# Optimization experiments

Hardware: AMD Instinct MI355X
Metric: run time of the kernel (lower is better)

The kernel has to match this reference:

```python
import jax, jax.numpy as jnp
import numpy as np

B, N = 32, 1024
CD, GD, HD, OD = 896, 384, 256, 1280  # cluster/geometric/hidden/output dims
EPS_BN = 1e-5


def _w(k, out_d, in_d):
    return jax.random.normal(k, (in_d, out_d), jnp.float32) / np.sqrt(in_d)


def setup_inputs() -> dict:
    key = jax.random.key(0)
    ks = jax.random.split(key, 12)
    return {
        "cluster_features": jax.random.normal(ks[0], (B, N, CD), jnp.float32),
        "geometric_features": jax.random.normal(ks[1], (B, N, GD), jnp.float32),
        "cluster_weights": jax.random.uniform(ks[2], (B, N, N), jnp.float32),
        # linear projections (stored as [in, out])
        "Wq": _w(ks[3], HD, CD), "bq": jnp.zeros((HD,), jnp.float32),
        "Wk": _w(ks[4], HD, GD), "bk": jnp.zeros((HD,), jnp.float32),
        "Wv": _w(ks[5], HD, GD), "bv": jnp.zeros((HD,), jnp.float32),
        "Wcp": _w(ks[6], OD // 2, CD), "bcp": jnp.zeros((OD // 2,), jnp.float32),
        "Wgp": _w(ks[7], OD // 2, HD), "bgp": jnp.zeros((OD // 2,), jnp.float32),
        # fusion head: Linear -> BN(eval) -> ReLU -> (Dropout=identity) -> Linear
        "Wf1": _w(ks[8], OD, OD), "bf1": jnp.zeros((OD,), jnp.float32),
        "bn_gamma": jnp.ones((OD,), jnp.float32),
        "bn_beta": jnp.zeros((OD,), jnp.float32),
        "bn_mean": jnp.zeros((OD,), jnp.float32),
        "bn_var": jnp.ones((OD,), jnp.float32),
        "Wf2": _w(ks[9], OD, OD), "bf2": jnp.zeros((OD,), jnp.float32),
    }


def reference(cluster_features, geometric_features, cluster_weights,
              Wq, bq, Wk, bk, Wv, bv, Wcp, bcp, Wgp, bgp,
              Wf1, bf1, bn_gamma, bn_beta, bn_mean, bn_var, Wf2, bf2):
    Q = cluster_features @ Wq + bq            # [B,N,HD]
    K = geometric_features @ Wk + bk          # [B,N,HD]
    V = geometric_features @ Wv + bv          # [B,N,HD]

    scale = 1.0 / np.sqrt(Q.shape[-1]).astype(np.float32)
    scores = jnp.einsum('bnd,bmd->bnm', Q, K) * scale  # [B,N,N]
    scores = scores + jnp.log(cluster_weights + 1e-8)
    attn = jax.nn.softmax(scores, axis=-1)             # [B,N,N]
    attended = jnp.einsum('bnm,bmd->bnd', attn, V)     # [B,N,HD]

    cluster_pooled = jnp.mean(cluster_features, axis=1)  # [B,CD]
    geom_pooled = jnp.mean(attended, axis=1)             # [B,HD]

    combined = jnp.concatenate([cluster_pooled @ Wcp + bcp,
                                geom_pooled @ Wgp + bgp], axis=-1)  # [B,OD]

    h = combined @ Wf1 + bf1
    h = (h - bn_mean) * jax.lax.rsqrt(bn_var + EPS_BN) * bn_gamma + bn_beta  # BN eval
    h = jax.nn.relu(h)  # dropout is identity at inference
    out = h @ Wf2 + bf2
    return out, attn
```

## Files before the change

### kernel.cpp

```cpp
#include <hip/hip_runtime.h>
#include <stdint.h>

typedef short    v8s  __attribute__((ext_vector_type(8)));
typedef float    v4f  __attribute__((ext_vector_type(4)));
typedef unsigned short u16x8 __attribute__((ext_vector_type(8)));
typedef unsigned short ushort_t;

#define NB   32
#define NN   1024
#define CD   896
#define GD   384
#define HD   256
#define OD   1280
#define SP   1028

static __device__ __forceinline__ unsigned short f2bf(float f) {
    union { float f; unsigned u; } v; v.f = f;
    unsigned r = v.u + 0x7fffu + ((v.u >> 16) & 1u);
    return (unsigned short)(r >> 16);
}

static __device__ __forceinline__ v4f mfma16(v8s a, v8s b, v4f c) {
    return __builtin_amdgcn_mfma_f32_16x16x32_bf16(a, b, c, 0, 0, 0);
}

static __device__ __forceinline__ void stage_cvt16(const float* __restrict__ src, ushort_t* dst) {
    const float4* s4 = (const float4*)src;
    float4 f0 = s4[0], f1 = s4[1], f2 = s4[2], f3 = s4[3];
    u16x8 p0, p1;
    p0[0]=f2bf(f0.x); p0[1]=f2bf(f0.y); p0[2]=f2bf(f0.z); p0[3]=f2bf(f0.w);
    p0[4]=f2bf(f1.x); p0[5]=f2bf(f1.y); p0[6]=f2bf(f1.z); p0[7]=f2bf(f1.w);
    p1[0]=f2bf(f2.x); p1[1]=f2bf(f2.y); p1[2]=f2bf(f2.z); p1[3]=f2bf(f2.w);
    p1[4]=f2bf(f3.x); p1[5]=f2bf(f3.y); p1[6]=f2bf(f3.z); p1[7]=f2bf(f3.w);
    *(u16x8*)dst = p0;
    *(u16x8*)(dst + 8) = p1;
}

static __device__ __forceinline__ void stage_copy16(const ushort_t* __restrict__ src, ushort_t* dst) {
    const u16x8* s = (const u16x8*)src;
    u16x8 a = s[0], b = s[1];
    *(u16x8*)dst = a;
    *(u16x8*)(dst + 8) = b;
}

__global__ void convw_kernel(const float* __restrict__ W, ushort_t* __restrict__ Wt, int Kd) {
    int idx = blockIdx.x * 256 + threadIdx.x;
    int k = idx >> 8, n = idx & 255;
    Wt[(size_t)n * Kd + k] = f2bf(W[idx]);
}

__global__ void zero_kernel(float* __restrict__ p, int n) {
    int i = blockIdx.x * 256 + threadIdx.x;
    if (i < n) p[i] = 0.f;
}

__global__ void pool_kernel(const float* __restrict__ cf, float* __restrict__ pooled) {
    int b = blockIdx.y, chunk = blockIdx.x, t = threadIdx.x;
    if (t >= 224) return;
    const float4* p = (const float4*)(cf + (size_t)(b * NN + chunk * 128) * CD) + t;
    float4 s = {0.f, 0.f, 0.f, 0.f};
    #pragma unroll 4
    for (int n = 0; n < 128; ++n) {
        float4 v = p[(size_t)n * 224];
        s.x += v.x; s.y += v.y; s.z += v.z; s.w += v.w;
    }
    const float sc = 1.f / 1024.f;
    float* dst = pooled + b * CD + t * 4;
    atomicAdd(dst + 0, s.x * sc);
    atomicAdd(dst + 1, s.y * sc);
    atomicAdd(dst + 2, s.z * sc);
    atomicAdd(dst + 3, s.w * sc);
}

template<int KD>
__global__ __launch_bounds__(256) void proj_kernel(
    const float* __restrict__ A, const ushort_t* __restrict__ Wt,
    const float* __restrict__ bias, ushort_t* __restrict__ C)
{
    __shared__ ushort_t lA[128 * 40];
    __shared__ ushort_t lB[128 * 40];
    const int tid  = threadIdx.x;
    const int m0   = blockIdx.x * 128;
    const int n0   = blockIdx.y * 128;
    const int lane = tid & 63, wave = tid >> 6;
    const int l15  = lane & 15, quad = lane >> 4;
    const int wrow = (wave >> 1) * 64, wcol = (wave & 1) * 64;
    const int srow = tid >> 1, shalf = tid & 1;

    v4f acc[4][4];
    #pragma unroll
    for (int i = 0; i < 4; ++i)
        #pragma unroll
        for (int j = 0; j < 4; ++j) acc[i][j] = v4f{0.f, 0.f, 0.f, 0.f};

    for (int kt = 0; kt < KD / 32; ++kt) {
        stage_cvt16(A + (size_t)(m0 + srow) * KD + kt * 32 + shalf * 16,
                    &lA[srow * 40 + shalf * 16]);
        stage_copy16(Wt + (size_t)(n0 + srow) * KD + kt * 32 + shalf * 16,
                     &lB[srow * 40 + shalf * 16]);
        __syncthreads();
        v8s af[4], bfr[4];
        #pragma unroll
        for (int rt = 0; rt < 4; ++rt) af[rt]  = *(const v8s*)&lA[(wrow + rt * 16 + l15) * 40 + quad * 8];
        #pragma unroll
        for (int ct = 0; ct < 4; ++ct) bfr[ct] = *(const v8s*)&lB[(wcol + ct * 16 + l15) * 40 + quad * 8];
        #pragma unroll
        for (int rt = 0; rt < 4; ++rt)
            #pragma unroll
            for (int ct = 0; ct < 4; ++ct)
                acc[rt][ct] = mfma16(af[rt], bfr[ct], acc[rt][ct]);
        __syncthreads();
    }

    #pragma unroll
    for (int ct = 0; ct < 4; ++ct) {
        int col = n0 + wcol + ct * 16 + l15;
        float bv = bias[col];
        #pragma unroll
        for (int rt = 0; rt < 4; ++rt)
            #pragma unroll
            for (int r = 0; r < 4; ++r) {
                int row = m0 + wrow + rt * 16 + quad * 4 + r;
                C[(size_t)row * 256 + col] = f2bf(acc[rt][ct][r] + bv);
            }
    }
}

__global__ __launch_bounds__(512) void attn_kernel(
    const ushort_t* __restrict__ Qb, const ushort_t* __restrict__ Kb,
    const float* __restrict__ cw,
    float* __restrict__ attn, float* __restrict__ colsum)
{
    __shared__ float S[32 * SP];
    const int bat = blockIdx.x;
    const int m0  = blockIdx.y * 32;
    const int tid = threadIdx.x;
    const int lane = tid & 63, wave = tid >> 6;
    const int l15 = lane & 15, quad = lane >> 4;

    v8s af[2][8];
    #pragma unroll
    for (int rt = 0; rt < 2; ++rt)
        #pragma unroll
        for (int ks = 0; ks < 8; ++ks)
            af[rt][ks] = *(const v8s*)(Qb + (size_t)(bat * NN + m0 + rt * 16 + l15) * HD + ks * 32 + quad * 8);

    const int n0w = wave * 128;
    #pragma unroll 2
    for (int ct = 0; ct < 8; ++ct) {
        const int col = n0w + ct * 16 + l15;
        v8s bfr[8];
        #pragma unroll
        for (int ks = 0; ks < 8; ++ks)
            bfr[ks] = *(const v8s*)(Kb + (size_t)(bat * NN + col) * HD + ks * 32 + quad * 8);
        float w0[4], w1[4];
        const size_t cwb = ((size_t)bat << 20) + col;
        #pragma unroll
        for (int r = 0; r < 4; ++r) {
            w0[r] = cw[cwb + (size_t)(m0 + quad * 4 + r) * NN];
            w1[r] = cw[cwb + (size_t)(m0 + 16 + quad * 4 + r) * NN];
        }
        v4f acc0 = {0.f, 0.f, 0.f, 0.f}, acc1 = {0.f, 0.f, 0.f, 0.f};
        #pragma unroll
        for (int ks = 0; ks < 8; ++ks) {
            acc0 = mfma16(af[0][ks], bfr[ks], acc0);
            acc1 = mfma16(af[1][ks], bfr[ks], acc1);
        }
        #pragma unroll
        for (int r = 0; r < 4; ++r) {
            const int row0 = quad * 4 + r;
            S[row0 * SP + col]        = acc0[r] * 0.0625f + __logf(w0[r] + 1e-8f);
            S[(16 + row0) * SP + col] = acc1[r] * 0.0625f + __logf(w1[r] + 1e-8f);
        }
    }
    __syncthreads();

    float4 cs[4];
    #pragma unroll
    for (int i = 0; i < 4; ++i) cs[i] = float4{0.f, 0.f, 0.f, 0.f};

    #pragma unroll 1
    for (int rr = 0; rr < 4; ++rr) {
        const int row = wave * 4 + rr;
        float* Srow = &S[row * SP];
        float4 v[4];
        #pragma unroll
        for (int i = 0; i < 4; ++i) v[i] = *(float4*)(Srow + i * 256 + lane * 4);
        float m = -1e30f;
        #pragma unroll
        for (int i = 0; i < 4; ++i)
            m = fmaxf(m, fmaxf(fmaxf(v[i].x, v[i].y), fmaxf(v[i].z, v[i].w)));
        #pragma unroll
        for (int off = 1; off <= 32; off <<= 1) m = fmaxf(m, __shfl_xor(m, off));
        float s = 0.f;
        #pragma unroll
        for (int i = 0; i < 4; ++i) {
            v[i].x = __expf(v[i].x - m); v[i].y = __expf(v[i].y - m);
            v[i].z = __expf(v[i].z - m); v[i].w = __expf(v[i].w - m);
            s += v[i].x + v[i].y + v[i].z + v[i].w;
        }
        #pragma unroll
        for (int off = 1; off <= 32; off <<= 1) s += __shfl_xor(s, off);
        const float inv = 1.0f / s;
        float* grow = attn + ((size_t)bat << 20) + (size_t)(m0 + row) * NN;
        #pragma unroll
        for (int i = 0; i < 4; ++i) {
            v[i].x *= inv; v[i].y *= inv; v[i].z *= inv; v[i].w *= inv;
            *(float4*)(grow + i * 256 + lane * 4) = v[i];
            cs[i].x += v[i].x; cs[i].y += v[i].y; cs[i].z += v[i].z; cs[i].w += v[i].w;
        }
    }

    __syncthreads();
    #pragma unroll
    for (int i = 0; i < 4; ++i)
        *(float4*)&S[wave * 1024 + i * 256 + lane * 4] = cs[i];
    __syncthreads();
    {
        const int c = tid * 2;
        float s0 = 0.f, s1 = 0.f;
        #pragma unroll
        for (int w = 0; w < 8; ++w) {
            float2 p = *(const float2*)&S[w * 1024 + c];
            s0 += p.x; s1 += p.y;
        }
        atomicAdd(&colsum[(size_t)bat * NN + c + 0], s0);
        atomicAdd(&colsum[(size_t)bat * NN + c + 1], s1);
    }
}

__global__ __launch_bounds__(192) void wpool_kernel(
    const float* __restrict__ gf, const float* __restrict__ colsum,
    float* __restrict__ gws)
{
    const int b = blockIdx.y, m0 = blockIdx.x * 128, t = threadIdx.x;
    const float2* base = (const float2*)(gf + (size_t)(b * NN + m0) * GD);
    const float* wbase = colsum + (size_t)b * NN + m0;
    float sx = 0.f, sy = 0.f;
    #pragma unroll 4
    for (int m = 0; m < 128; ++m) {
        const float w = wbase[m] * (1.f / 1024.f);
        float2 v = base[(size_t)m * (GD / 2) + t];
        sx += w * v.x; sy += w * v.y;
    }
    atomicAdd(&gws[b * GD + 2 * t + 0], sx);
    atomicAdd(&gws[b * GD + 2 * t + 1], sy);
}

__global__ __launch_bounds__(256) void vproj_kernel(
    const float* __restrict__ gws, const float* __restrict__ Wv,
    const float* __restrict__ bv, float* __restrict__ gpool)
{
    const int b = blockIdx.x, d = threadIdx.x;
    const float* g = gws + (size_t)b * GD;
    float acc = bv[d];
    #pragma unroll 8
    for (int k = 0; k < GD; ++k) acc += g[k] * Wv[(size_t)k * HD + d];
    gpool[b * HD + d] = acc;
}

__global__ void tail1_kernel(const float* __restrict__ pooled, const float* __restrict__ gpool,
                             const float* __restrict__ Wcp, const float* __restrict__ bcp,
                             const float* __restrict__ Wgp, const float* __restrict__ bgp,
                             float* __restrict__ combined)
{
    int idx = blockIdx.x * 256 + threadIdx.x;
    int b = idx / OD, c = idx % OD;
    float acc;
    if (c < 640) {
        acc = bcp[c];
        const float* a = pooled + b * CD;
        for (int k = 0; k < CD; ++k) acc += a[k] * Wcp[k * 640 + c];
    } else {
        int c2 = c - 640;
        acc = bgp[c2];
        const float* g = gpool + b * HD;
        for (int k = 0; k < HD; ++k) acc += g[k] * Wgp[k * 640 + c2];
    }
    combined[idx] = acc;
}

__global__ void tail2_kernel(const float* __restrict__ combined, const float* __restrict__ Wf1,
                             const float* __restrict__ bf1,
                             const float* __restrict__ g, const float* __restrict__ be,
                             const float* __restrict__ mn, const float* __restrict__ vr,
                             float* __restrict__ h)
{
    int idx = blockIdx.x * 256 + threadIdx.x;
    int b = idx / OD, c = idx % OD;
    float acc = bf1[c];
    const float* a = combined + b * OD;
    for (int k = 0; k < OD; ++k) acc += a[k] * Wf1[k * OD + c];
    float x = (acc - mn[c]) * rsqrtf(vr[c] + 1e-5f) * g[c] + be[c];
    h[idx] = fmaxf(x, 0.f);
}

__global__ void tail3_kernel(const float* __restrict__ h, const float* __restrict__ Wf2,
                             const float* __restrict__ bf2, float* __restrict__ out)
{
    int idx = blockIdx.x * 256 + threadIdx.x;
    int b = idx / OD, c = idx % OD;
    float acc = bf2[c];
    const float* a = h + b * OD;
    for (int k = 0; k < OD; ++k) acc += a[k] * Wf2[k * OD + c];
    out[idx] = acc;
}

extern "C" void kernel_launch(void* const* d_in, const int* in_sizes, int n_in,
                              void* d_out, int out_size, void* d_ws, size_t ws_size,
                              hipStream_t stream)
{
    const float* cf  = (const float*)d_in[0];
    const float* gf  = (const float*)d_in[1];
    const float* cw  = (const float*)d_in[2];
    const float* Wq  = (const float*)d_in[3];  const float* bq  = (const float*)d_in[4];
    const float* Wk  = (const float*)d_in[5];  const float* bk  = (const float*)d_in[6];
    const float* Wv  = (const float*)d_in[7];  const float* bv  = (const float*)d_in[8];
    const float* Wcp = (const float*)d_in[9];  const float* bcp = (const float*)d_in[10];
    const float* Wgp = (const float*)d_in[11]; const float* bgp = (const float*)d_in[12];
    const float* Wf1 = (const float*)d_in[13]; const float* bf1 = (const float*)d_in[14];
    const float* bng = (const float*)d_in[15]; const float* bnb = (const float*)d_in[16];
    const float* bnm = (const float*)d_in[17]; const float* bnv = (const float*)d_in[18];
    const float* Wf2 = (const float*)d_in[19]; const float* bf2 = (const float*)d_in[20];

    float* out  = (float*)d_out;
    float* attn = out + NB * OD;

    char* w = (char*)d_ws;
    ushort_t* Qb  = (ushort_t*)w; w += (size_t)NB * NN * HD * 2;
    ushort_t* Kb  = (ushort_t*)w; w += (size_t)NB * NN * HD * 2;
    ushort_t* Wqt = (ushort_t*)w; w += (size_t)HD * CD * 2;
    ushort_t* Wkt = (ushort_t*)w; w += (size_t)HD * GD * 2;
    float* pooled   = (float*)w; w += (size_t)NB * CD * 4;
    float* gpool    = (float*)w; w += (size_t)NB * HD * 4;
    float* colsum   = (float*)w; w += (size_t)NB * NN * 4;
    float* gws      = (float*)w; w += (size_t)NB * GD * 4;
    float* combined = (float*)w; w += (size_t)NB * OD * 4;
    float* hbuf     = (float*)w; w += (size_t)NB * OD * 4;

    const int nz = NB * (CD + HD + NN + GD);
    zero_kernel<<<dim3((nz + 255) / 256), dim3(256), 0, stream>>>(pooled, nz);
    convw_kernel<<<dim3(CD), dim3(256), 0, stream>>>(Wq, Wqt, CD);
    convw_kernel<<<dim3(GD), dim3(256), 0, stream>>>(Wk, Wkt, GD);
    pool_kernel<<<dim3(8, 32), dim3(256), 0, stream>>>(cf, pooled);

    proj_kernel<CD><<<dim3(256, 2), dim3(256), 0, stream>>>(cf, Wqt, bq, Qb);
    proj_kernel<GD><<<dim3(256, 2), dim3(256), 0, stream>>>(gf, Wkt, bk, Kb);

    attn_kernel<<<dim3(32, 32), dim3(512), 0, stream>>>(Qb, Kb, cw, attn, colsum);

    wpool_kernel<<<dim3(8, 32), dim3(192), 0, stream>>>(gf, colsum, gws);
    vproj_kernel<<<dim3(32), dim3(256), 0, stream>>>(gws, Wv, bv, gpool);

    tail1_kernel<<<dim3(160), dim3(256), 0, stream>>>(pooled, gpool, Wcp, bcp, Wgp, bgp, combined);
    tail2_kernel<<<dim3(160), dim3(256), 0, stream>>>(combined, Wf1, bf1, bng, bnb, bnm, bnv, hbuf);
    tail3_kernel<<<dim3(160), dim3(256), 0, stream>>>(hbuf, Wf2, bf2, out);
}
```

Baseline: 754.8 us.

## Keep attention scores in registers and add ILP to reduction kernels

The attention kernel no longer stages the 32x1024 score tile in a ~128KB shared buffer. Each 256-thread block now handles 16 rows, keeps all scores in MFMA accumulators, preloads the log-weights into them, and does max and sum through shuffles plus a tiny shared reduction. The point is higher occupancy and fewer LDS round trips. The cost is that attn stores become strided 4-byte writes instead of float4 rows, and colsum atomics rise to one per column per block. Separately, the pool, wpool, vproj and tail kernels split their sums across multiple accumulators for more ILP, and pool uses twice as many blocks.

```diff
diff --git a/kernel.cpp b/kernel.cpp
--- a/kernel.cpp
+++ b/kernel.cpp
@@ -12,7 +12,6 @@
 #define GD   384
 #define HD   256
 #define OD   1280
-#define SP   1028
 
 static __device__ __forceinline__ unsigned short f2bf(float f) {
     union { float f; unsigned u; } v; v.f = f;
@@ -57,19 +56,25 @@
 __global__ void pool_kernel(const float* __restrict__ cf, float* __restrict__ pooled) {
     int b = blockIdx.y, chunk = blockIdx.x, t = threadIdx.x;
     if (t >= 224) return;
-    const float4* p = (const float4*)(cf + (size_t)(b * NN + chunk * 128) * CD) + t;
-    float4 s = {0.f, 0.f, 0.f, 0.f};
-    #pragma unroll 4
-    for (int n = 0; n < 128; ++n) {
-        float4 v = p[(size_t)n * 224];
-        s.x += v.x; s.y += v.y; s.z += v.z; s.w += v.w;
+    const float4* p = (const float4*)(cf + (size_t)(b * NN + chunk * 64) * CD) + t;
+    float4 s0{0,0,0,0}, s1{0,0,0,0}, s2{0,0,0,0}, s3{0,0,0,0};
+    #pragma unroll 1
+    for (int n = 0; n < 64; n += 4) {
+        float4 v0 = p[(size_t)(n + 0) * 224];
+        float4 v1 = p[(size_t)(n + 1) * 224];
+        float4 v2 = p[(size_t)(n + 2) * 224];
+        float4 v3 = p[(size_t)(n + 3) * 224];
+        s0.x += v0.x; s0.y += v0.y; s0.z += v0.z; s0.w += v0.w;
+        s1.x += v1.x; s1.y += v1.y; s1.z += v1.z; s1.w += v1.w;
+        s2.x += v2.x; s2.y += v2.y; s2.z += v2.z; s2.w += v2.w;
+        s3.x += v3.x; s3.y += v3.y; s3.z += v3.z; s3.w += v3.w;
     }
     const float sc = 1.f / 1024.f;
     float* dst = pooled + b * CD + t * 4;
-    atomicAdd(dst + 0, s.x * sc);
-    atomicAdd(dst + 1, s.y * sc);
-    atomicAdd(dst + 2, s.z * sc);
-    atomicAdd(dst + 3, s.w * sc);
+    atomicAdd(dst + 0, (s0.x + s1.x + s2.x + s3.x) * sc);
+    atomicAdd(dst + 1, (s0.y + s1.y + s2.y + s3.y) * sc);
+    atomicAdd(dst + 2, (s0.z + s1.z + s2.z + s3.z) * sc);
+    atomicAdd(dst + 3, (s0.w + s1.w + s2.w + s3.w) * sc);
 }
 
 template<int KD>
@@ -126,106 +131,109 @@
     }
 }
 
-__global__ __launch_bounds__(512) void attn_kernel(
+__global__ __launch_bounds__(256, 4) void attn_kernel(
     const ushort_t* __restrict__ Qb, const ushort_t* __restrict__ Kb,
     const float* __restrict__ cw,
     float* __restrict__ attn, float* __restrict__ colsum)
 {
-    __shared__ float S[32 * SP];
+    __shared__ float red[2][4][16];
     const int bat = blockIdx.x;
-    const int m0  = blockIdx.y * 32;
+    const int m0  = blockIdx.y * 16;
     const int tid = threadIdx.x;
     const int lane = tid & 63, wave = tid >> 6;
     const int l15 = lane & 15, quad = lane >> 4;
-
-    v8s af[2][8];
-    #pragma unroll
-    for (int rt = 0; rt < 2; ++rt)
-        #pragma unroll
-        for (int ks = 0; ks < 8; ++ks)
-            af[rt][ks] = *(const v8s*)(Qb + (size_t)(bat * NN + m0 + rt * 16 + l15) * HD + ks * 32 + quad * 8);
-
-    const int n0w = wave * 128;
-    #pragma unroll 2
-    for (int ct = 0; ct < 8; ++ct) {
+    const int n0w = wave * 256;
+
+    v4f acc[16];
+    const float* cwp = cw + ((size_t)bat << 20);
+    #pragma unroll
+    for (int ct = 0; ct < 16; ++ct) {
         const int col = n0w + ct * 16 + l15;
-        v8s bfr[8];
-        #pragma unroll
-        for (int ks = 0; ks < 8; ++ks)
-            bfr[ks] = *(const v8s*)(Kb + (size_t)(bat * NN + col) * HD + ks * 32 + quad * 8);
-        float w0[4], w1[4];
-        const size_t cwb = ((size_t)bat << 20) + col;
         #pragma unroll
         for (int r = 0; r < 4; ++r) {
-            w0[r] = cw[cwb + (size_t)(m0 + quad * 4 + r) * NN];
-            w1[r] = cw[cwb + (size_t)(m0 + 16 + quad * 4 + r) * NN];
-        }
-        v4f acc0 = {0.f, 0.f, 0.f, 0.f}, acc1 = {0.f, 0.f, 0.f, 0.f};
-        #pragma unroll
-        for (int ks = 0; ks < 8; ++ks) {
-            acc0 = mfma16(af[0][ks], bfr[ks], acc0);
-            acc1 = mfma16(af[1][ks], bfr[ks], acc1);
-        }
+            float w = cwp[(size_t)(m0 + quad * 4 + r) * NN + col];
+            acc[ct][r] = 16.f * __logf(w + 1e-8f);
+        }
+    }
+
+    const ushort_t* qrow = Qb + (size_t)(bat * NN + m0 + l15) * HD + quad * 8;
+    const ushort_t* krow = Kb + (size_t)(bat * NN + n0w + l15) * HD + quad * 8;
+    #pragma unroll 1
+    for (int ks = 0; ks < 8; ++ks) {
+        v8s af = *(const v8s*)(qrow + ks * 32);
+        #pragma unroll
+        for (int ct = 0; ct < 16; ++ct) {
+            v8s bf = *(const v8s*)(krow + (size_t)(ct * 16) * HD + ks * 32);
+            acc[ct] = mfma16(af, bf, acc[ct]);
+        }
+    }
+
+    #pragma unroll
+    for (int ct = 0; ct < 16; ++ct)
+        #pragma unroll
+        for (int r = 0; r < 4; ++r) acc[ct][r] *= 0.0625f;
+
+    float mr[4];
+    #pragma unroll
+    for (int r = 0; r < 4; ++r) {
+        float m = acc[0][r];
+        #pragma unroll
+        for (int ct = 1; ct < 16; ++ct) m = fmaxf(m, acc[ct][r]);
+        #pragma unroll
+        for (int off = 1; off <= 8; off <<= 1) m = fmaxf(m, __shfl_xor(m, off));
+        mr[r] = m;
+    }
+    if (l15 == 0) {
+        #pragma unroll
+        for (int r = 0; r < 4; ++r) red[0][wave][quad * 4 + r] = mr[r];
+    }
+    __syncthreads();
+    #pragma unroll
+    for (int r = 0; r < 4; ++r) {
+        const int row = quad * 4 + r;
+        mr[r] = fmaxf(fmaxf(red[0][0][row], red[0][1][row]),
+                      fmaxf(red[0][2][row], red[0][3][row]));
+    }
+
+    float sr[4];
+    #pragma unroll
+    for (int r = 0; r < 4; ++r) {
+        float s = 0.f;
+        #pragma unroll
+        for (int ct = 0; ct < 16; ++ct) {
+            float p = __expf(acc[ct][r] - mr[r]);
+            acc[ct][r] = p;
+            s += p;
+        }
+        #pragma unroll
+        for (int off = 1; off <= 8; off <<= 1) s += __shfl_xor(s, off);
+        sr[r] = s;
+    }
+    if (l15 == 0) {
+        #pragma unroll
+        for (int r = 0; r < 4; ++r) red[1][wave][quad * 4 + r] = sr[r];
+    }
+    __syncthreads();
+    #pragma unroll
+    for (int r = 0; r < 4; ++r) {
+        const int row = quad * 4 + r;
+        sr[r] = 1.0f / (red[1][0][row] + red[1][1][row] + red[1][2][row] + red[1][3][row]);
+    }
+
+    float* abase = attn + ((size_t)bat << 20) + (size_t)m0 * NN;
+    #pragma unroll
+    for (int ct = 0; ct < 16; ++ct) {
+        const int col = n0w + ct * 16 + l15;
+        float c = 0.f;
         #pragma unroll
         for (int r = 0; r < 4; ++r) {
-            const int row0 = quad * 4 + r;
-            S[row0 * SP + col]        = acc0[r] * 0.0625f + __logf(w0[r] + 1e-8f);
-            S[(16 + row0) * SP + col] = acc1[r] * 0.0625f + __logf(w1[r] + 1e-8f);
-        }
-    }
-    __syncthreads();
-
-    float4 cs[4];
-    #pragma unroll
-    for (int i = 0; i < 4; ++i) cs[i] = float4{0.f, 0.f, 0.f, 0.f};
-
-    #pragma unroll 1
-    for (int rr = 0; rr < 4; ++rr) {
-        const int row = wave * 4 + rr;
-        float* Srow = &S[row * SP];
-        float4 v[4];
-        #pragma unroll
-        for (int i = 0; i < 4; ++i) v[i] = *(float4*)(Srow + i * 256 + lane * 4);
-        float m = -1e30f;
-        #pragma unroll
-        for (int i = 0; i < 4; ++i)
-            m = fmaxf(m, fmaxf(fmaxf(v[i].x, v[i].y), fmaxf(v[i].z, v[i].w)));
-        #pragma unroll
-        for (int off = 1; off <= 32; off <<= 1) m = fmaxf(m, __shfl_xor(m, off));
-        float s = 0.f;
-        #pragma unroll
-        for (int i = 0; i < 4; ++i) {
-            v[i].x = __expf(v[i].x - m); v[i].y = __expf(v[i].y - m);
-            v[i].z = __expf(v[i].z - m); v[i].w = __expf(v[i].w - m);
-            s += v[i].x + v[i].y + v[i].z + v[i].w;
-        }
-        #pragma unroll
-        for (int off = 1; off <= 32; off <<= 1) s += __shfl_xor(s, off);
-        const float inv = 1.0f / s;
-        float* grow = attn + ((size_t)bat << 20) + (size_t)(m0 + row) * NN;
-        #pragma unroll
-        for (int i = 0; i < 4; ++i) {
-            v[i].x *= inv; v[i].y *= inv; v[i].z *= inv; v[i].w *= inv;
-            *(float4*)(grow + i * 256 + lane * 4) = v[i];
-            cs[i].x += v[i].x; cs[i].y += v[i].y; cs[i].z += v[i].z; cs[i].w += v[i].w;
-        }
-    }
-
-    __syncthreads();
-    #pragma unroll
-    for (int i = 0; i < 4; ++i)
-        *(float4*)&S[wave * 1024 + i * 256 + lane * 4] = cs[i];
-    __syncthreads();
-    {
-        const int c = tid * 2;
-        float s0 = 0.f, s1 = 0.f;
-        #pragma unroll
-        for (int w = 0; w < 8; ++w) {
-            float2 p = *(const float2*)&S[w * 1024 + c];
-            s0 += p.x; s1 += p.y;
-        }
-        atomicAdd(&colsum[(size_t)bat * NN + c + 0], s0);
-        atomicAdd(&colsum[(size_t)bat * NN + c + 1], s1);
+            float p = acc[ct][r] * sr[r];
+            abase[(size_t)(quad * 4 + r) * NN + col] = p;
+            c += p;
+        }
+        c += __shfl_xor(c, 16);
+        c += __shfl_xor(c, 32);
+        if (quad == 0) atomicAdd(&colsum[(size_t)bat * NN + col], c);
     }
 }
 
@@ -236,15 +244,22 @@
     const int b = blockIdx.y, m0 = blockIdx.x * 128, t = threadIdx.x;
     const float2* base = (const float2*)(gf + (size_t)(b * NN + m0) * GD);
     const float* wbase = colsum + (size_t)b * NN + m0;
-    float sx = 0.f, sy = 0.f;
-    #pragma unroll 4
-    for (int m = 0; m < 128; ++m) {
-        const float w = wbase[m] * (1.f / 1024.f);
-        float2 v = base[(size_t)m * (GD / 2) + t];
-        sx += w * v.x; sy += w * v.y;
-    }
-    atomicAdd(&gws[b * GD + 2 * t + 0], sx);
-    atomicAdd(&gws[b * GD + 2 * t + 1], sy);
+    const float sc = 1.f / 1024.f;
+    float sx0 = 0.f, sy0 = 0.f, sx1 = 0.f, sy1 = 0.f;
+    float sx2 = 0.f, sy2 = 0.f, sx3 = 0.f, sy3 = 0.f;
+    #pragma unroll 1
+    for (int m = 0; m < 128; m += 4) {
+        float w0 = wbase[m + 0] * sc; float2 v0 = base[(size_t)(m + 0) * (GD / 2) + t];
+        float w1 = wbase[m + 1] * sc; float2 v1 = base[(size_t)(m + 1) * (GD / 2) + t];
+        float w2 = wbase[m + 2] * sc; float2 v2 = base[(size_t)(m + 2) * (GD / 2) + t];
+        float w3 = wbase[m + 3] * sc; float2 v3 = base[(size_t)(m + 3) * (GD / 2) + t];
+        sx0 += w0 * v0.x; sy0 += w0 * v0.y;
+        sx1 += w1 * v1.x; sy1 += w1 * v1.y;
+        sx2 += w2 * v2.x; sy2 += w2 * v2.y;
+        sx3 += w3 * v3.x; sy3 += w3 * v3.y;
+    }
+    atomicAdd(&gws[b * GD + 2 * t + 0], (sx0 + sx1) + (sx2 + sx3));
+    atomicAdd(&gws[b * GD + 2 * t + 1], (sy0 + sy1) + (sy2 + sy3));
 }
 
 __global__ __launch_bounds__(256) void vproj_kernel(
@@ -253,10 +268,15 @@
 {
     const int b = blockIdx.x, d = threadIdx.x;
     const float* g = gws + (size_t)b * GD;
-    float acc = bv[d];
-    #pragma unroll 8
-    for (int k = 0; k < GD; ++k) acc += g[k] * Wv[(size_t)k * HD + d];
-    gpool[b * HD + d] = acc;
+    float a0 = 0.f, a1 = 0.f, a2 = 0.f, a3 = 0.f;
+    #pragma unroll 2
+    for (int k = 0; k < GD; k += 4) {
+        a0 += g[k + 0] * Wv[(size_t)(k + 0) * HD + d];
+        a1 += g[k + 1] * Wv[(size_t)(k + 1) * HD + d];
+        a2 += g[k + 2] * Wv[(size_t)(k + 2) * HD + d];
+        a3 += g[k + 3] * Wv[(size_t)(k + 3) * HD + d];
+    }
+    gpool[b * HD + d] = bv[d] + (a0 + a1) + (a2 + a3);
 }
 
 __global__ void tail1_kernel(const float* __restrict__ pooled, const float* __restrict__ gpool,
@@ -266,18 +286,32 @@
 {
     int idx = blockIdx.x * 256 + threadIdx.x;
     int b = idx / OD, c = idx % OD;
-    float acc;
+    float a0 = 0.f, a1 = 0.f, a2 = 0.f, a3 = 0.f, bias;
     if (c < 640) {
-        acc = bcp[c];
+        bias = bcp[c];
         const float* a = pooled + b * CD;
-        for (int k = 0; k < CD; ++k) acc += a[k] * Wcp[k * 640 + c];
+        #pragma unroll 1
+        for (int k = 0; k < CD; k += 4) {
+            float4 av = *(const float4*)(a + k);
+            a0 += av.x * Wcp[(size_t)(k + 0) * 640 + c];
+            a1 += av.y * Wcp[(size_t)(k + 1) * 640 + c];
+            a2 += av.z * Wcp[(size_t)(k + 2) * 640 + c];
+            a3 += av.w * Wcp[(size_t)(k + 3) * 640 + c];
+        }
     } else {
         int c2 = c - 640;
-        acc = bgp[c2];
+        bias = bgp[c2];
         const float* g = gpool + b * HD;
-        for (int k = 0; k < HD; ++k) acc += g[k] * Wgp[k * 640 + c2];
-    }
-    combined[idx] = acc;
+        #pragma unroll 1
+        for (int k = 0; k < HD; k += 4) {
+            float4 gv = *(const float4*)(g + k);
+            a0 += gv.x * Wgp[(size_t)(k + 0) * 640 + c2];
+            a1 += gv.y * Wgp[(size_t)(k + 1) * 640 + c2];
+            a2 += gv.z * Wgp[(size_t)(k + 2) * 640 + c2];
+            a3 += gv.w * Wgp[(size_t)(k + 3) * 640 + c2];
+        }
+    }
+    combined[idx] = bias + (a0 + a1) + (a2 + a3);
 }
 
 __global__ void tail2_kernel(const float* __restrict__ combined, const float* __restrict__ Wf1,
@@ -288,9 +322,17 @@
 {
     int idx = blockIdx.x * 256 + threadIdx.x;
     int b = idx / OD, c = idx % OD;
-    float acc = bf1[c];
     const float* a = combined + b * OD;
-    for (int k = 0; k < OD; ++k) acc += a[k] * Wf1[k * OD + c];
+    float a0 = 0.f, a1 = 0.f, a2 = 0.f, a3 = 0.f;
+    #pragma unroll 1
+    for (int k = 0; k < OD; k += 4) {
+        float4 av = *(const float4*)(a + k);
+        a0 += av.x * Wf1[(size_t)(k + 0) * OD + c];
+        a1 += av.y * Wf1[(size_t)(k + 1) * OD + c];
+        a2 += av.z * Wf1[(size_t)(k + 2) * OD + c];
+        a3 += av.w * Wf1[(size_t)(k + 3) * OD + c];
+    }
+    float acc = bf1[c] + (a0 + a1) + (a2 + a3);
     float x = (acc - mn[c]) * rsqrtf(vr[c] + 1e-5f) * g[c] + be[c];
     h[idx] = fmaxf(x, 0.f);
 }
@@ -300,10 +342,17 @@
 {
     int idx = blockIdx.x * 256 + threadIdx.x;
     int b = idx / OD, c = idx % OD;
-    float acc = bf2[c];
     const float* a = h + b * OD;
-    for (int k = 0; k < OD; ++k) acc += a[k] * Wf2[k * OD + c];
-    out[idx] = acc;
+    float a0 = 0.f, a1 = 0.f, a2 = 0.f, a3 = 0.f;
+    #pragma unroll 1
+    for (int k = 0; k < OD; k += 4) {
+        float4 av = *(const float4*)(a + k);
+        a0 += av.x * Wf2[(size_t)(k + 0) * OD + c];
+        a1 += av.y * Wf2[(size_t)(k + 1) * OD + c];
+        a2 += av.z * Wf2[(size_t)(k + 2) * OD + c];
+        a3 += av.w * Wf2[(size_t)(k + 3) * OD + c];
+    }
+    out[idx] = bf2[c] + (a0 + a1) + (a2 + a3);
 }
 
 extern "C" void kernel_launch(void* const* d_in, const int* in_sizes, int n_in,
@@ -342,12 +391,12 @@
     zero_kernel<<<dim3((nz + 255) / 256), dim3(256), 0, stream>>>(pooled, nz);
     convw_kernel<<<dim3(CD), dim3(256), 0, stream>>>(Wq, Wqt, CD);
     convw_kernel<<<dim3(GD), dim3(256), 0, stream>>>(Wk, Wkt, GD);
-    pool_kernel<<<dim3(8, 32), dim3(256), 0, stream>>>(cf, pooled);
+    pool_kernel<<<dim3(16, 32), dim3(256), 0, stream>>>(cf, pooled);
 
     proj_kernel<CD><<<dim3(256, 2), dim3(256), 0, stream>>>(cf, Wqt, bq, Qb);
     proj_kernel<GD><<<dim3(256, 2), dim3(256), 0, stream>>>(gf, Wkt, bk, Kb);
 
-    attn_kernel<<<dim3(32, 32), dim3(512), 0, stream>>>(Qb, Kb, cw, attn, colsum);
+    attn_kernel<<<dim3(32, 64), dim3(256), 0, stream>>>(Qb, Kb, cw, attn, colsum);
 
     wpool_kernel<<<dim3(8, 32), dim3(192), 0, stream>>>(gf, colsum, gws);
     vproj_kernel<<<dim3(32), dim3(256), 0, stream>>>(gws, Wv, bv, gpool);
```

After: 1.004 ms. 33.1% more time.

## Split-K tail GEMVs with atomics, widen projection tiles, finer pooling grid

Applied to the files above, without the earlier changes.

The three small tail matmuls are split along K across extra grid rows and accumulate with atomicAdd into zeroed buffers, with BN+ReLU moved to its own kernel. This gives the tail more blocks than the previous 160-block serial-K launches. The projection kernel now uses 512 threads and covers all 256 output columns per block, so each A tile is converted once instead of twice. The pooling kernel uses a 4x larger grid with multiple accumulators. The cost is extra zeroing, atomic traffic and one more launch.

```diff
diff --git a/kernel.cpp b/kernel.cpp
--- a/kernel.cpp
+++ b/kernel.cpp
@@ -57,34 +57,39 @@
 __global__ void pool_kernel(const float* __restrict__ cf, float* __restrict__ pooled) {
     int b = blockIdx.y, chunk = blockIdx.x, t = threadIdx.x;
     if (t >= 224) return;
-    const float4* p = (const float4*)(cf + (size_t)(b * NN + chunk * 128) * CD) + t;
-    float4 s = {0.f, 0.f, 0.f, 0.f};
-    #pragma unroll 4
-    for (int n = 0; n < 128; ++n) {
-        float4 v = p[(size_t)n * 224];
-        s.x += v.x; s.y += v.y; s.z += v.z; s.w += v.w;
+    const float4* p = (const float4*)(cf + (size_t)(b * NN + chunk * 32) * CD) + t;
+    float4 s0{0,0,0,0}, s1{0,0,0,0}, s2{0,0,0,0}, s3{0,0,0,0};
+    #pragma unroll 1
+    for (int n = 0; n < 32; n += 4) {
+        float4 v0 = p[(size_t)(n + 0) * 224];
+        float4 v1 = p[(size_t)(n + 1) * 224];
+        float4 v2 = p[(size_t)(n + 2) * 224];
+        float4 v3 = p[(size_t)(n + 3) * 224];
+        s0.x += v0.x; s0.y += v0.y; s0.z += v0.z; s0.w += v0.w;
+        s1.x += v1.x; s1.y += v1.y; s1.z += v1.z; s1.w += v1.w;
+        s2.x += v2.x; s2.y += v2.y; s2.z += v2.z; s2.w += v2.w;
+        s3.x += v3.x; s3.y += v3.y; s3.z += v3.z; s3.w += v3.w;
     }
     const float sc = 1.f / 1024.f;
     float* dst = pooled + b * CD + t * 4;
-    atomicAdd(dst + 0, s.x * sc);
-    atomicAdd(dst + 1, s.y * sc);
-    atomicAdd(dst + 2, s.z * sc);
-    atomicAdd(dst + 3, s.w * sc);
+    atomicAdd(dst + 0, (s0.x + s1.x + s2.x + s3.x) * sc);
+    atomicAdd(dst + 1, (s0.y + s1.y + s2.y + s3.y) * sc);
+    atomicAdd(dst + 2, (s0.z + s1.z + s2.z + s3.z) * sc);
+    atomicAdd(dst + 3, (s0.w + s1.w + s2.w + s3.w) * sc);
 }
 
 template<int KD>
-__global__ __launch_bounds__(256) void proj_kernel(
+__global__ __launch_bounds__(512, 4) void proj_kernel(
     const float* __restrict__ A, const ushort_t* __restrict__ Wt,
     const float* __restrict__ bias, ushort_t* __restrict__ C)
 {
     __shared__ ushort_t lA[128 * 40];
-    __shared__ ushort_t lB[128 * 40];
+    __shared__ ushort_t lB[256 * 40];
     const int tid  = threadIdx.x;
     const int m0   = blockIdx.x * 128;
-    const int n0   = blockIdx.y * 128;
     const int lane = tid & 63, wave = tid >> 6;
     const int l15  = lane & 15, quad = lane >> 4;
-    const int wrow = (wave >> 1) * 64, wcol = (wave & 1) * 64;
+    const int wrow = (wave >> 2) * 64, wcol = (wave & 3) * 64;
     const int srow = tid >> 1, shalf = tid & 1;
 
     v4f acc[4][4];
@@ -94,9 +99,10 @@
         for (int j = 0; j < 4; ++j) acc[i][j] = v4f{0.f, 0.f, 0.f, 0.f};
 
     for (int kt = 0; kt < KD / 32; ++kt) {
-        stage_cvt16(A + (size_t)(m0 + srow) * KD + kt * 32 + shalf * 16,
-                    &lA[srow * 40 + shalf * 16]);
-        stage_copy16(Wt + (size_t)(n0 + srow) * KD + kt * 32 + shalf * 16,
+        if (tid < 256)
+            stage_cvt16(A + (size_t)(m0 + srow) * KD + kt * 32 + shalf * 16,
+                        &lA[srow * 40 + shalf * 16]);
+        stage_copy16(Wt + (size_t)srow * KD + kt * 32 + shalf * 16,
                      &lB[srow * 40 + shalf * 16]);
         __syncthreads();
         v8s af[4], bfr[4];
@@ -114,7 +120,7 @@
 
     #pragma unroll
     for (int ct = 0; ct < 4; ++ct) {
-        int col = n0 + wcol + ct * 16 + l15;
+        int col = wcol + ct * 16 + l15;
         float bv = bias[col];
         #pragma unroll
         for (int rt = 0; rt < 4; ++rt)
@@ -266,32 +272,42 @@
 {
     int idx = blockIdx.x * 256 + threadIdx.x;
     int b = idx / OD, c = idx % OD;
-    float acc;
+    int kc = blockIdx.y;
+    float acc = 0.f;
     if (c < 640) {
-        acc = bcp[c];
+        if (kc == 0) acc = bcp[c];
         const float* a = pooled + b * CD;
-        for (int k = 0; k < CD; ++k) acc += a[k] * Wcp[k * 640 + c];
+        const int k0 = kc * 224;
+        for (int k = k0; k < k0 + 224; ++k) acc += a[k] * Wcp[k * 640 + c];
     } else {
         int c2 = c - 640;
-        acc = bgp[c2];
+        if (kc == 0) acc = bgp[c2];
         const float* g = gpool + b * HD;
-        for (int k = 0; k < HD; ++k) acc += g[k] * Wgp[k * 640 + c2];
-    }
-    combined[idx] = acc;
+        const int k0 = kc * 64;
+        for (int k = k0; k < k0 + 64; ++k) acc += g[k] * Wgp[k * 640 + c2];
+    }
+    atomicAdd(&combined[idx], acc);
 }
 
 __global__ void tail2_kernel(const float* __restrict__ combined, const float* __restrict__ Wf1,
-                             const float* __restrict__ bf1,
-                             const float* __restrict__ g, const float* __restrict__ be,
-                             const float* __restrict__ mn, const float* __restrict__ vr,
-                             float* __restrict__ h)
+                             const float* __restrict__ bf1, float* __restrict__ h)
 {
     int idx = blockIdx.x * 256 + threadIdx.x;
     int b = idx / OD, c = idx % OD;
-    float acc = bf1[c];
+    int k0 = blockIdx.y * 256;
+    float acc = (blockIdx.y == 0) ? bf1[c] : 0.f;
     const float* a = combined + b * OD;
-    for (int k = 0; k < OD; ++k) acc += a[k] * Wf1[k * OD + c];
-    float x = (acc - mn[c]) * rsqrtf(vr[c] + 1e-5f) * g[c] + be[c];
+    for (int k = k0; k < k0 + 256; ++k) acc += a[k] * Wf1[k * OD + c];
+    atomicAdd(&h[idx], acc);
+}
+
+__global__ void bnrelu_kernel(float* __restrict__ h,
+                              const float* __restrict__ g, const float* __restrict__ be,
+                              const float* __restrict__ mn, const float* __restrict__ vr)
+{
+    int idx = blockIdx.x * 256 + threadIdx.x;
+    int c = idx % OD;
+    float x = (h[idx] - mn[c]) * rsqrtf(vr[c] + 1e-5f) * g[c] + be[c];
     h[idx] = fmaxf(x, 0.f);
 }
 
@@ -300,10 +316,11 @@
 {
     int idx = blockIdx.x * 256 + threadIdx.x;
     int b = idx / OD, c = idx % OD;
-    float acc = bf2[c];
+    int k0 = blockIdx.y * 256;
+    float acc = (blockIdx.y == 0) ? bf2[c] : 0.f;
     const float* a = h + b * OD;
-    for (int k = 0; k < OD; ++k) acc += a[k] * Wf2[k * OD + c];
-    out[idx] = acc;
+    for (int k = k0; k < k0 + 256; ++k) acc += a[k] * Wf2[k * OD + c];
+    atomicAdd(&out[idx], acc);
 }
 
 extern "C" void kernel_launch(void* const* d_in, const int* in_sizes, int n_in,
@@ -338,21 +355,23 @@
     float* combined = (float*)w; w += (size_t)NB * OD * 4;
     float* hbuf     = (float*)w; w += (size_t)NB * OD * 4;
 
-    const int nz = NB * (CD + HD + NN + GD);
+    const int nz = NB * (CD + HD + NN + GD + OD + OD);
     zero_kernel<<<dim3((nz + 255) / 256), dim3(256), 0, stream>>>(pooled, nz);
+    zero_kernel<<<dim3((NB * OD + 255) / 256), dim3(256), 0, stream>>>(out, NB * OD);
     convw_kernel<<<dim3(CD), dim3(256), 0, stream>>>(Wq, Wqt, CD);
     convw_kernel<<<dim3(GD), dim3(256), 0, stream>>>(Wk, Wkt, GD);
-    pool_kernel<<<dim3(8, 32), dim3(256), 0, stream>>>(cf, pooled);
-
-    proj_kernel<CD><<<dim3(256, 2), dim3(256), 0, stream>>>(cf, Wqt, bq, Qb);
-    proj_kernel<GD><<<dim3(256, 2), dim3(256), 0, stream>>>(gf, Wkt, bk, Kb);
+    pool_kernel<<<dim3(32, 32), dim3(256), 0, stream>>>(cf, pooled);
+
+    proj_kernel<CD><<<dim3(256), dim3(512), 0, stream>>>(cf, Wqt, bq, Qb);
+    proj_kernel<GD><<<dim3(256), dim3(512), 0, stream>>>(gf, Wkt, bk, Kb);
 
     attn_kernel<<<dim3(32, 32), dim3(512), 0, stream>>>(Qb, Kb, cw, attn, colsum);
 
     wpool_kernel<<<dim3(8, 32), dim3(192), 0, stream>>>(gf, colsum, gws);
     vproj_kernel<<<dim3(32), dim3(256), 0, stream>>>(gws, Wv, bv, gpool);
 
-    tail1_kernel<<<dim3(160), dim3(256), 0, stream>>>(pooled, gpool, Wcp, bcp, Wgp, bgp, combined);
-    tail2_kernel<<<dim3(160), dim3(256), 0, stream>>>(combined, Wf1, bf1, bng, bnb, bnm, bnv, hbuf);
-    tail3_kernel<<<dim3(160), dim3(256), 0, stream>>>(hbuf, Wf2, bf2, out);
-}
+    tail1_kernel<<<dim3(160, 4), dim3(256), 0, stream>>>(pooled, gpool, Wcp, bcp, Wgp, bgp, combined);
+    tail2_kernel<<<dim3(160, 5), dim3(256), 0, stream>>>(combined, Wf1, bf1, hbuf);
+    bnrelu_kernel<<<dim3(160), dim3(256), 0, stream>>>(hbuf, bng, bnb, bnm, bnv);
+    tail3_kernel<<<dim3(160, 5), dim3(256), 0, stream>>>(hbuf, Wf2, bf2, out);
+}
```

Result: faster. 690.4 us (-8.5%).
